# Optimization experiments

Measured on AMD Instinct MI355X. Metric: run time of the kernel, lower is better.

The kernel has to match this reference:

```python
import jax, jax.numpy as jnp
import numpy as np

B, L, D = 4, 896, 2048
HQ, HKV, HD = 32, 8, 64
GROUP = HQ // HKV          # 4
TOKENS_PER_FRAME = 7
ROPE_BASE = 10000.0


def setup_inputs() -> dict:
    key = jax.random.key(0)
    ks = jax.random.split(key, 5)
    s = 0.02
    return {
        "x": jax.random.normal(ks[0], (B, L, D), jnp.float32),
        "wq": jax.random.normal(ks[1], (D, D), jnp.float32) * s,
        "wk": jax.random.normal(ks[2], (D, HKV * HD), jnp.float32) * s,
        "wv": jax.random.normal(ks[3], (D, HKV * HD), jnp.float32) * s,
        "wo": jax.random.normal(ks[4], (D, D), jnp.float32) * s,
        "pos_ids": jnp.arange(L, dtype=jnp.int32),
    }


def _apply_rotary(t, cos, sin):
    # t: [B, L, H, HD]; rotate all HD dims, interleaved pairs.
    Bt, Lt, Ht, Hd = t.shape
    tp = t.reshape(Bt, Lt, Ht, Hd // 2, 2)
    x1, x2 = tp[..., 0], tp[..., 1]
    c = cos[None, :, None, :]   # [1, L, 1, HD/2]
    s = sin[None, :, None, :]
    y1 = x1 * c - x2 * s
    y2 = x1 * s + x2 * c
    return jnp.stack([y1, y2], axis=-1).reshape(Bt, Lt, Ht, Hd)


def reference(x, wq, wk, wv, wo, pos_ids):
    Bx, Lx, Dx = x.shape
    q = (x @ wq).reshape(Bx, Lx, HQ, HD)
    k = (x @ wk).reshape(Bx, Lx, HKV, HD)
    v = (x @ wv).reshape(Bx, Lx, HKV, HD)

    # RoPE (rot_dim = head_dim), scale = 1.0
    half = HD // 2
    inv_freq = 1.0 / (ROPE_BASE ** (jnp.arange(half, dtype=jnp.float32) / half))
    freqs = pos_ids.astype(jnp.float32)[:, None] * inv_freq[None, :]  # [L, HD/2]
    cos, sin = jnp.cos(freqs), jnp.sin(freqs)
    q = _apply_rotary(q, cos, sin)
    k = _apply_rotary(k, cos, sin)

    # GQA: expand kv heads to q heads (kv_head = q_head // GROUP)
    k = jnp.repeat(k, GROUP, axis=2)   # [B, L, HQ, HD]
    v = jnp.repeat(v, GROUP, axis=2)

    scale = 1.0 / jnp.sqrt(jnp.float32(HD))
    scores = jnp.einsum('blhd,bmhd->bhlm', q, k) * scale  # [B, HQ, L, L]

    # frame-block causal mask: allow key frame <= query frame
    pos = jnp.arange(Lx)
    fid = pos // TOKENS_PER_FRAME
    allow = fid[None, :] <= fid[:, None]                  # [L, L]
    neg = jnp.finfo(scores.dtype).min
    scores = jnp.where(allow[None, None], scores, neg)

    probs = jax.nn.softmax(scores, axis=-1)
    out = jnp.einsum('bhlm,bmhd->blhd', probs, v).reshape(Bx, Lx, Dx)
    return out @ wo
```

## Files before the change

### kernel.cpp

```cpp
#include <hip/hip_runtime.h>
#include <hip/hip_bf16.h>
#include <cstdint>

typedef __bf16 bf16;
typedef __bf16 bf16x8 __attribute__((ext_vector_type(8)));
typedef float floatx4 __attribute__((ext_vector_type(4)));

#define B_   4
#define L_   896
#define D_   2048
#define HQ_  32
#define HKV_ 8
#define HD_  64
#define NQKV 3072
#define M_   3584

__device__ inline void gl_lds16(const bf16* g, bf16* l) {
    __builtin_amdgcn_global_load_lds(
        (const __attribute__((address_space(1))) void*)g,
        (__attribute__((address_space(3))) void*)l, 16, 0, 0);
}

__global__ __launch_bounds__(256) void convert_to_bf16(const float* __restrict__ in,
                                                       bf16* __restrict__ out) {
    long q = (long)blockIdx.x * 256 + threadIdx.x;
    float4 v = ((const float4*)in)[q];
    union { bf16 b[4]; ushort4 u; } w;
    w.b[0] = (bf16)v.x; w.b[1] = (bf16)v.y; w.b[2] = (bf16)v.z; w.b[3] = (bf16)v.w;
    ((ushort4*)out)[q] = w.u;
}

__global__ __launch_bounds__(256) void rope_cs_kernel(const int* __restrict__ pos_ids,
                                                      float2* __restrict__ cs) {
    int idx = blockIdx.x * 256 + threadIdx.x;
    if (idx >= L_ * 32) return;
    int l = idx >> 5, i = idx & 31;
    float p = (float)pos_ids[l];
    float inv = exp2f(-(float)i * (13.287712379549449f / 32.0f));
    float a = p * inv;
    cs[idx] = make_float2(cosf(a), sinf(a));
}

__global__ __launch_bounds__(256) void rope_apply(bf16* __restrict__ QKV,
                                                  const float2* __restrict__ cs) {
    int idx = blockIdx.x * 256 + threadIdx.x;
    int m = idx / 320, g = idx - m * 320;
    int l = m % L_;
    int hp = (g * 4) & 31;
    const float2* ct = &cs[l * 32 + hp];
    bf16* p = QKV + (long)m * NQKV + g * 8;
    bf16x8 v = *(bf16x8*)p;
    bf16x8 w;
#pragma unroll
    for (int i = 0; i < 4; i++) {
        float2 csv = ct[i];
        float x1 = (float)v[2 * i], x2 = (float)v[2 * i + 1];
        w[2 * i]     = (bf16)(x1 * csv.x - x2 * csv.y);
        w[2 * i + 1] = (bf16)(x1 * csv.y + x2 * csv.x);
    }
    *(bf16x8*)p = w;
}

__global__ __launch_bounds__(256) void transpose_cvt(
    const float* __restrict__ in, ushort* __restrict__ out, int C, int R) {
    __shared__ ushort t[64][72];
    int tid = threadIdx.x;
    int tr = tid >> 4, tc = (tid & 15) << 2;
    long r0 = (long)blockIdx.y << 6, c0 = (long)blockIdx.x << 6;
#pragma unroll
    for (int i = 0; i < 4; ++i) {
        float4 v = *(const float4*)&in[(r0 + tr + i * 16) * C + c0 + tc];
        union { bf16 b[4]; ushort4 u; } w;
        w.b[0] = (bf16)v.x; w.b[1] = (bf16)v.y; w.b[2] = (bf16)v.z; w.b[3] = (bf16)v.w;
        *(ushort4*)&t[tr + i * 16][tc] = w.u;
    }
    __syncthreads();
#pragma unroll
    for (int i = 0; i < 4; ++i) {
        ushort4 w;
        w.x = t[tc + 0][tr + i * 16];
        w.y = t[tc + 1][tr + i * 16];
        w.z = t[tc + 2][tr + i * 16];
        w.w = t[tc + 3][tr + i * 16];
        *(ushort4*)&out[(c0 + tr + i * 16) * R + r0 + tc] = w;
    }
}

__global__ __launch_bounds__(256) void transpose_u16(
    const ushort* __restrict__ in, ushort* __restrict__ out,
    int ld_in, int ld_out, long is1, long is2, long os1, long os2) {
    __shared__ ushort t[64][72];
    int z = blockIdx.z;
    const ushort* ip = in + (long)(z >> 3) * is1 + (long)(z & 7) * is2;
    ushort* op = out + (long)(z >> 3) * os1 + (long)(z & 7) * os2;
    int tid = threadIdx.x;
    int tr = tid >> 4, tc = (tid & 15) << 2;
    long r0 = (long)blockIdx.y << 6, c0 = (long)blockIdx.x << 6;
#pragma unroll
    for (int i = 0; i < 4; ++i) {
        ushort4 v = *(const ushort4*)&ip[(r0 + tr + i * 16) * ld_in + c0 + tc];
        *(ushort4*)&t[tr + i * 16][tc] = v;
    }
    __syncthreads();
#pragma unroll
    for (int i = 0; i < 4; ++i) {
        ushort4 w;
        w.x = t[tc + 0][tr + i * 16];
        w.y = t[tc + 1][tr + i * 16];
        w.z = t[tc + 2][tr + i * 16];
        w.w = t[tc + 3][tr + i * 16];
        *(ushort4*)&op[(c0 + tr + i * 16) * ld_out + r0 + tc] = w;
    }
}

__global__ __launch_bounds__(256) void gemm_bt(
    const bf16* __restrict__ A, const bf16* __restrict__ Bt, void* __restrict__ C,
    int Mtot, int Ntot, int Ktot, int outf32) {
    __shared__ bf16 As[128 * 32];
    __shared__ bf16 Bs[128 * 32];
    const int tid  = threadIdx.x;
    const int wid  = tid >> 6, lane = tid & 63;
    const int quad = lane >> 4, l16 = lane & 15;
    const int wm = (wid >> 1) << 6, wn = (wid & 1) << 6;
    const long m0 = (long)blockIdx.y << 7, n0 = (long)blockIdx.x << 7;
    const int srow = tid >> 2, scol = (tid & 3) << 3;

    floatx4 acc[4][4];
#pragma unroll
    for (int i = 0; i < 4; i++)
#pragma unroll
        for (int j = 0; j < 4; j++)
#pragma unroll
            for (int r = 0; r < 4; r++) acc[i][j][r] = 0.f;

    for (int k0 = 0; k0 < Ktot; k0 += 32) {
        __syncthreads();
        gl_lds16(&A[(m0 + srow) * Ktot + k0 + scol],       &As[tid * 8]);
        gl_lds16(&A[(m0 + srow + 64) * Ktot + k0 + scol],  &As[tid * 8 + 2048]);
        gl_lds16(&Bt[(n0 + srow) * Ktot + k0 + scol],      &Bs[tid * 8]);
        gl_lds16(&Bt[(n0 + srow + 64) * Ktot + k0 + scol], &Bs[tid * 8 + 2048]);
        __syncthreads();
        bf16x8 af[4], bfr[4];
#pragma unroll
        for (int i = 0; i < 4; i++) af[i]  = *(bf16x8*)&As[(wm + i * 16 + l16) * 32 + quad * 8];
#pragma unroll
        for (int j = 0; j < 4; j++) bfr[j] = *(bf16x8*)&Bs[(wn + j * 16 + l16) * 32 + quad * 8];
#pragma unroll
        for (int i = 0; i < 4; i++)
#pragma unroll
            for (int j = 0; j < 4; j++)
                acc[i][j] = __builtin_amdgcn_mfma_f32_16x16x32_bf16(af[i], bfr[j], acc[i][j], 0, 0, 0);
    }

#pragma unroll
    for (int j = 0; j < 4; j++) {
        const int n = (int)n0 + wn + j * 16 + l16;
#pragma unroll
        for (int i = 0; i < 4; i++) {
#pragma unroll
            for (int r = 0; r < 4; r++) {
                long m = m0 + wm + i * 16 + quad * 4 + r;
                if (outf32) ((float*)C)[m * Ntot + n] = acc[i][j][r];
                else        ((bf16*)C)[m * Ntot + n] = (bf16)acc[i][j][r];
            }
        }
    }
}

__global__ __launch_bounds__(256) void attn_kernel(
    const bf16* __restrict__ QKV,
    const bf16* __restrict__ Vt,
    bf16* __restrict__ AO) {
    __shared__ bf16 Ks[64 * 72];
    __shared__ bf16 Vs[64 * 72];
    __shared__ bf16 Ps[4][16 * 72];
    const int tid  = threadIdx.x;
    const int wid  = tid >> 6, lane = tid & 63;
    const int quad = lane >> 4, c = lane & 15;
    const int b = blockIdx.z, hq = blockIdx.y, kvh = hq >> 2;
    const int q0b = blockIdx.x * 64;
    const int q0 = q0b + wid * 16;
    bf16* ps = &Ps[wid][0];

    const bf16* Qb = QKV + ((long)(b * L_ + q0)) * NQKV + hq * HD_;
    const bf16* Kb = QKV + ((long)(b * L_)) * NQKV + D_ + kvh * HD_;
    const bf16* Vb = Vt + ((long)(b * HKV_ + kvh)) * (HD_ * L_);

    bf16x8 qf0 = *(const bf16x8*)&Qb[(long)c * NQKV + quad * 8];
    bf16x8 qf1 = *(const bf16x8*)&Qb[(long)c * NQKV + 32 + quad * 8];

    float lsum[4];
    floatx4 o[4];
#pragma unroll
    for (int r = 0; r < 4; r++) lsum[r] = 0.f;
#pragma unroll
    for (int nt = 0; nt < 4; nt++)
#pragma unroll
        for (int r = 0; r < 4; r++) o[nt][r] = 0.f;

    int fe[4];
#pragma unroll
    for (int r = 0; r < 4; r++) { int l = q0 + quad * 4 + r; fe[r] = (l / 7 + 1) * 7; }
    const int kend = ((q0b + 63) / 7 + 1) * 7;

    const int srow = tid >> 3, schunk = (tid & 7) << 3;

    for (int k0 = 0; k0 < kend; k0 += 64) {
        bf16x8 kg0 = *(const bf16x8*)&Kb[(long)(k0 + srow) * NQKV + schunk];
        bf16x8 kg1 = *(const bf16x8*)&Kb[(long)(k0 + 32 + srow) * NQKV + schunk];
        bf16x8 vg0 = *(const bf16x8*)&Vb[(long)srow * L_ + k0 + schunk];
        bf16x8 vg1 = *(const bf16x8*)&Vb[(long)(srow + 32) * L_ + k0 + schunk];
        __syncthreads();
        *(bf16x8*)&Ks[srow * 72 + schunk]        = kg0;
        *(bf16x8*)&Ks[(srow + 32) * 72 + schunk] = kg1;
        *(bf16x8*)&Vs[srow * 72 + schunk]        = vg0;
        *(bf16x8*)&Vs[(srow + 32) * 72 + schunk] = vg1;
        __syncthreads();

        floatx4 s[4];
#pragma unroll
        for (int n = 0; n < 4; n++) {
#pragma unroll
            for (int r = 0; r < 4; r++) s[n][r] = 0.f;
            bf16x8 kf0 = *(bf16x8*)&Ks[(n * 16 + c) * 72 + quad * 8];
            bf16x8 kf1 = *(bf16x8*)&Ks[(n * 16 + c) * 72 + 32 + quad * 8];
            s[n] = __builtin_amdgcn_mfma_f32_16x16x32_bf16(qf0, kf0, s[n], 0, 0, 0);
            s[n] = __builtin_amdgcn_mfma_f32_16x16x32_bf16(qf1, kf1, s[n], 0, 0, 0);
        }
#pragma unroll
        for (int n = 0; n < 4; n++) {
            const int key = k0 + n * 16 + c;
#pragma unroll
            for (int r = 0; r < 4; r++) {
                float e = __expf(fmaf(s[n][r], 0.125f, -12.0f));
                e = (key < fe[r]) ? e : 0.f;
                lsum[r] += e;
                ps[(quad * 4 + r) * 72 + n * 16 + c] = (bf16)e;
            }
        }
        bf16x8 pf0 = *(bf16x8*)&ps[c * 72 + quad * 8];
        bf16x8 pf1 = *(bf16x8*)&ps[c * 72 + 32 + quad * 8];
#pragma unroll
        for (int nt = 0; nt < 4; nt++) {
            bf16x8 vf0 = *(bf16x8*)&Vs[(nt * 16 + c) * 72 + quad * 8];
            bf16x8 vf1 = *(bf16x8*)&Vs[(nt * 16 + c) * 72 + 32 + quad * 8];
            o[nt] = __builtin_amdgcn_mfma_f32_16x16x32_bf16(pf0, vf0, o[nt], 0, 0, 0);
            o[nt] = __builtin_amdgcn_mfma_f32_16x16x32_bf16(pf1, vf1, o[nt], 0, 0, 0);
        }
    }
#pragma unroll
    for (int r = 0; r < 4; r++) {
#pragma unroll
        for (int off = 1; off < 16; off <<= 1) lsum[r] += __shfl_xor(lsum[r], off);
    }
#pragma unroll
    for (int nt = 0; nt < 4; nt++)
#pragma unroll
        for (int r = 0; r < 4; r++) {
            int l = q0 + quad * 4 + r;
            AO[((long)(b * L_ + l)) * D_ + hq * HD_ + nt * 16 + c] = (bf16)(o[nt][r] / lsum[r]);
        }
}

extern "C" void kernel_launch(void* const* d_in, const int* in_sizes, int n_in,
                              void* d_out, int out_size, void* d_ws, size_t ws_size,
                              hipStream_t stream) {
    (void)in_sizes; (void)n_in; (void)out_size; (void)ws_size;
    const float* x  = (const float*)d_in[0];
    const float* wq = (const float*)d_in[1];
    const float* wk = (const float*)d_in[2];
    const float* wv = (const float*)d_in[3];
    const float* wo = (const float*)d_in[4];
    const int* pos  = (const int*)d_in[5];

    bf16* ws    = (bf16*)d_ws;
    bf16* xb    = ws;
    bf16* wqkvT = ws + 7340032L;
    bf16* woT   = ws + 13631488L;
    bf16* QKV   = ws + 17825792L;
    bf16* Vt    = ws + 28835840L;
    bf16* AO    = xb;
    float2* cs  = (float2*)(ws + 30670848L);

    convert_to_bf16<<<dim3(7168), 256, 0, stream>>>(x, xb);
    rope_cs_kernel<<<dim3(112), dim3(256), 0, stream>>>(pos, cs);

    transpose_cvt<<<dim3(32, 32), 256, 0, stream>>>(wq, (ushort*)wqkvT, 2048, 2048);
    transpose_cvt<<<dim3(8, 32), 256, 0, stream>>>(wk, (ushort*)(wqkvT + 4194304L), 512, 2048);
    transpose_cvt<<<dim3(8, 32), 256, 0, stream>>>(wv, (ushort*)(wqkvT + 5242880L), 512, 2048);
    transpose_cvt<<<dim3(32, 32), 256, 0, stream>>>(wo, (ushort*)woT, 2048, 2048);

    gemm_bt<<<dim3(24, 28), 256, 0, stream>>>(xb, wqkvT, QKV, M_, NQKV, D_, 0);

    rope_apply<<<dim3(4480), 256, 0, stream>>>(QKV, cs);

    transpose_u16<<<dim3(1, 14, 32), 256, 0, stream>>>(
        (const ushort*)(QKV + 2560), (ushort*)Vt, 3072, 896,
        896L * 3072, 64, 8L * 57344, 57344);

    attn_kernel<<<dim3(14, 32, 4), 256, 0, stream>>>(QKV, Vt, AO);

    gemm_bt<<<dim3(16, 28), 256, 0, stream>>>(AO, woT, d_out, M_, D_, D_, 1);
}
```

Measured before the change: 305.8 us.

## Replace GEMM with 256x256 tiled, double-buffered, XCD-remapped 8-wave kernel

Replaces the 128x128, BK=32, single-buffered GEMM with a 256x256 tile kernel using 512 threads, BK=64 and double-buffered LDS staging through global_load_lds. LDS reads use a swizzled layout to avoid bank conflicts. Block indices are remapped so neighbouring tiles land on the same XCD, and each step is split into four MFMA phases with loads interleaved, priority raising and manual waitcnt/barriers. The aim is more data reuse per tile and loads overlapped with MFMA work. The cost is fewer workgroups for these shapes (168 and 112 blocks), which may underfill the 256 CUs, plus heavy register and LDS use.

Result: slower. 317.0 us (+3.7%).

```diff
diff --git a/kernel.cpp b/kernel.cpp
--- a/kernel.cpp
+++ b/kernel.cpp
@@ -19,6 +19,12 @@
     __builtin_amdgcn_global_load_lds(
         (const __attribute__((address_space(1))) void*)g,
         (__attribute__((address_space(3))) void*)l, 16, 0, 0);
+}
+
+__device__ inline void barrier_() {
+    asm volatile("" ::: "memory");
+    __builtin_amdgcn_s_barrier();
+    asm volatile("" ::: "memory");
 }
 
 __global__ __launch_bounds__(256) void convert_to_bf16(const float* __restrict__ in,
@@ -113,58 +119,155 @@
     }
 }
 
-__global__ __launch_bounds__(256) void gemm_bt(
+
+template <int RQ>
+__device__ inline void lda(const bf16* p, int l16, int colA, bf16x8 (&af)[4][2]) {
+#pragma unroll
+    for (int i = 0; i < 4; ++i)
+#pragma unroll
+        for (int ks = 0; ks < 2; ++ks)
+            af[i][ks] = *(const bf16x8*)&p[(RQ * 64 + i * 16 + l16) * 64 + ks * 32 + colA];
+}
+
+template <int CQ>
+__device__ inline void ldb(const bf16* p, int brow, int l16, int colA, bf16x8 (&bq)[2][2]) {
+#pragma unroll
+    for (int j = 0; j < 2; ++j)
+#pragma unroll
+        for (int ks = 0; ks < 2; ++ks)
+            bq[j][ks] = *(const bf16x8*)&p[(brow + (CQ * 2 + j) * 16 + l16) * 64 + ks * 32 + colA];
+}
+
+template <int RQ, int CQ>
+__device__ inline void mma(const bf16x8 (&af)[4][2], const bf16x8 (&bq)[2][2],
+                           floatx4 (&acc)[8][4]) {
+#pragma unroll
+    for (int i = 0; i < 4; ++i)
+#pragma unroll
+        for (int j = 0; j < 2; ++j) {
+            floatx4 c = acc[RQ * 4 + i][CQ * 2 + j];
+            c = __builtin_amdgcn_mfma_f32_16x16x32_bf16(af[i][0], bq[j][0], c, 0, 0, 0);
+            c = __builtin_amdgcn_mfma_f32_16x16x32_bf16(af[i][1], bq[j][1], c, 0, 0, 0);
+            acc[RQ * 4 + i][CQ * 2 + j] = c;
+        }
+}
+
+__device__ inline void stage_half(const bf16* gsrc, bf16* ldst, long rowK) {
+    gl_lds16(gsrc,            ldst);
+    gl_lds16(gsrc + 8 * rowK, ldst + 512);
+}
+
+__global__ __launch_bounds__(512, 2) void gemm256(
     const bf16* __restrict__ A, const bf16* __restrict__ Bt, void* __restrict__ C,
-    int Mtot, int Ntot, int Ktot, int outf32) {
-    __shared__ bf16 As[128 * 32];
-    __shared__ bf16 Bs[128 * 32];
-    const int tid  = threadIdx.x;
-    const int wid  = tid >> 6, lane = tid & 63;
+    int Ntot, int Ktot, int outf32) {
+    __shared__ bf16 lds[2][2][2][128 * 64];
+    const int tid = threadIdx.x;
+    const int w = tid >> 6, lane = tid & 63;
     const int quad = lane >> 4, l16 = lane & 15;
-    const int wm = (wid >> 1) << 6, wn = (wid & 1) << 6;
-    const long m0 = (long)blockIdx.y << 7, n0 = (long)blockIdx.x << 7;
-    const int srow = tid >> 2, scol = (tid & 3) << 3;
-
-    floatx4 acc[4][4];
-#pragma unroll
-    for (int i = 0; i < 4; i++)
-#pragma unroll
-        for (int j = 0; j < 4; j++)
-#pragma unroll
-            for (int r = 0; r < 4; r++) acc[i][j][r] = 0.f;
-
-    for (int k0 = 0; k0 < Ktot; k0 += 32) {
-        __syncthreads();
-        gl_lds16(&A[(m0 + srow) * Ktot + k0 + scol],       &As[tid * 8]);
-        gl_lds16(&A[(m0 + srow + 64) * Ktot + k0 + scol],  &As[tid * 8 + 2048]);
-        gl_lds16(&Bt[(n0 + srow) * Ktot + k0 + scol],      &Bs[tid * 8]);
-        gl_lds16(&Bt[(n0 + srow + 64) * Ktot + k0 + scol], &Bs[tid * 8 + 2048]);
-        __syncthreads();
-        bf16x8 af[4], bfr[4];
-#pragma unroll
-        for (int i = 0; i < 4; i++) af[i]  = *(bf16x8*)&As[(wm + i * 16 + l16) * 32 + quad * 8];
-#pragma unroll
-        for (int j = 0; j < 4; j++) bfr[j] = *(bf16x8*)&Bs[(wn + j * 16 + l16) * 32 + quad * 8];
-#pragma unroll
-        for (int i = 0; i < 4; i++)
-#pragma unroll
-            for (int j = 0; j < 4; j++)
-                acc[i][j] = __builtin_amdgcn_mfma_f32_16x16x32_bf16(af[i], bfr[j], acc[i][j], 0, 0, 0);
-    }
-
-#pragma unroll
-    for (int j = 0; j < 4; j++) {
-        const int n = (int)n0 + wn + j * 16 + l16;
-#pragma unroll
-        for (int i = 0; i < 4; i++) {
-#pragma unroll
-            for (int r = 0; r < 4; r++) {
-                long m = m0 + wm + i * 16 + quad * 4 + r;
-                if (outf32) ((float*)C)[m * Ntot + n] = acc[i][j][r];
-                else        ((bf16*)C)[m * Ntot + n] = (bf16)acc[i][j][r];
+    const int wr = w >> 2, wc = w & 3;
+
+    const int gx = gridDim.x;
+    const int nwg = gx * gridDim.y;
+    int orig = blockIdx.y * gx + blockIdx.x;
+    int q8 = nwg >> 3, r8 = nwg & 7;
+    int xcd = orig & 7, lid = orig >> 3;
+    int wg = (xcd < r8 ? xcd * (q8 + 1) : r8 * (q8 + 1) + (xcd - r8) * q8) + lid;
+    const long m0 = (long)(wg / gx) << 8;
+    const long n0 = (long)(wg % gx) << 8;
+
+    const long rowK = Ktot;
+    const int sl = lane ^ ((lane & 32) >> 4);
+    const int srow = w * 16 + (sl >> 3);
+    const int scol = (sl & 7) * 8;
+    const bf16* baseA = A  + (m0 + srow) * rowK + scol;
+    const bf16* baseB = Bt + (n0 + srow) * rowK + scol;
+    const int d0 = w * 1024 + lane * 8;
+
+    const int cswz = (l16 & 4) << 2;
+    const int colA = (quad * 8) ^ cswz;
+    const int brow = (wc & 1) * 64;
+
+    floatx4 acc[8][4];
+#pragma unroll
+    for (int i = 0; i < 8; ++i)
+#pragma unroll
+        for (int j = 0; j < 4; ++j)
+#pragma unroll
+            for (int r = 0; r < 4; ++r) acc[i][j][r] = 0.f;
+
+    bf16x8 af[4][2], bq0[2][2], bq1[2][2];
+
+    const int T = Ktot >> 6;
+    stage_half(baseA,                   &lds[0][0][0][d0], rowK);
+    stage_half(baseA + 128 * rowK,      &lds[0][0][1][d0], rowK);
+    stage_half(baseB,                   &lds[0][1][0][d0], rowK);
+    stage_half(baseB + 128 * rowK,      &lds[0][1][1][d0], rowK);
+    stage_half(baseB + 64,              &lds[1][1][0][d0], rowK);
+    stage_half(baseB + 128 * rowK + 64, &lds[1][1][1][d0], rowK);
+    asm volatile("s_waitcnt vmcnt(4)" ::: "memory");
+    barrier_();
+
+    for (int t = 0; t < T; ++t) {
+        const int cur = t & 1, nxt = cur ^ 1;
+        const bf16* pa = &lds[cur][0][wr][0];
+        const bf16* pb = &lds[cur][1][wc >> 1][0];
+        const long koff  = (long)(t + 1) * 64;
+        const long koff2 = (long)(t + 2) * 64;
+
+        lda<0>(pa, l16, colA, af);
+        ldb<0>(pb, brow, l16, colA, bq0);
+        if (t + 1 < T) stage_half(baseA + koff, &lds[nxt][0][0][d0], rowK);
+        barrier_();
+        asm volatile("s_waitcnt lgkmcnt(0)" ::: "memory");
+        __builtin_amdgcn_sched_barrier(0);
+        __builtin_amdgcn_s_setprio(1);
+        mma<0, 0>(af, bq0, acc);
+        __builtin_amdgcn_s_setprio(0);
+        barrier_();
+
+        ldb<1>(pb, brow, l16, colA, bq1);
+        if (t + 1 < T) stage_half(baseA + 128 * rowK + koff, &lds[nxt][0][1][d0], rowK);
+        barrier_();
+        asm volatile("s_waitcnt lgkmcnt(0)" ::: "memory");
+        __builtin_amdgcn_sched_barrier(0);
+        __builtin_amdgcn_s_setprio(1);
+        mma<0, 1>(af, bq1, acc);
+        __builtin_amdgcn_s_setprio(0);
+        barrier_();
+
+        lda<1>(pa, l16, colA, af);
+        if (t + 2 < T) stage_half(baseB + koff2, &lds[cur][1][0][d0], rowK);
+        barrier_();
+        asm volatile("s_waitcnt lgkmcnt(0)" ::: "memory");
+        __builtin_amdgcn_sched_barrier(0);
+        __builtin_amdgcn_s_setprio(1);
+        mma<1, 0>(af, bq0, acc);
+        __builtin_amdgcn_s_setprio(0);
+        barrier_();
+
+        if (t + 2 < T) stage_half(baseB + 128 * rowK + koff2, &lds[cur][1][1][d0], rowK);
+        barrier_();
+        asm volatile("s_waitcnt lgkmcnt(0)" ::: "memory");
+        __builtin_amdgcn_sched_barrier(0);
+        __builtin_amdgcn_s_setprio(1);
+        mma<1, 1>(af, bq1, acc);
+        __builtin_amdgcn_s_setprio(0);
+        if (t + 2 < T) asm volatile("s_waitcnt vmcnt(4)" ::: "memory");
+        else           asm volatile("s_waitcnt vmcnt(0)" ::: "memory");
+        barrier_();
+    }
+
+#pragma unroll
+    for (int ri = 0; ri < 8; ++ri)
+#pragma unroll
+        for (int j = 0; j < 4; ++j)
+#pragma unroll
+            for (int r = 0; r < 4; ++r) {
+                long m = m0 + wr * 128 + ri * 16 + quad * 4 + r;
+                long n = n0 + wc * 64 + j * 16 + l16;
+                if (outf32) ((float*)C)[m * Ntot + n] = acc[ri][j][r];
+                else        ((bf16*)C)[m * Ntot + n] = (bf16)acc[ri][j][r];
             }
-        }
-    }
 }
 
 __global__ __launch_bounds__(256) void attn_kernel(
@@ -290,7 +393,7 @@
     transpose_cvt<<<dim3(8, 32), 256, 0, stream>>>(wv, (ushort*)(wqkvT + 5242880L), 512, 2048);
     transpose_cvt<<<dim3(32, 32), 256, 0, stream>>>(wo, (ushort*)woT, 2048, 2048);
 
-    gemm_bt<<<dim3(24, 28), 256, 0, stream>>>(xb, wqkvT, QKV, M_, NQKV, D_, 0);
+    gemm256<<<dim3(12, 14), 512, 0, stream>>>(xb, wqkvT, QKV, NQKV, D_, 0);
 
     rope_apply<<<dim3(4480), 256, 0, stream>>>(QKV, cs);
 
@@ -300,5 +403,5 @@
 
     attn_kernel<<<dim3(14, 32, 4), 256, 0, stream>>>(QKV, Vt, AO);
 
-    gemm_bt<<<dim3(16, 28), 256, 0, stream>>>(AO, woT, d_out, M_, D_, D_, 1);
-}
+    gemm256<<<dim3(8, 14), 512, 0, stream>>>(AO, woT, d_out, D_, D_, 1);
+}
```
